# Optimization experiments

Measured on AMD Instinct MI355X. Metric: run time of the kernel, lower is better.

Reference implementation:

```python
import jax, jax.numpy as jnp
import numpy as np
from jax import lax

B, L, D, H = 2, 4096, 1024, 16
K = 4            # short conv kernel size
HD = D // H      # head dim = 64
EPS = 1e-5


def causal_dw_conv(x, w):
    # depthwise causal conv: x [B,L,D], w [D,K]
    xp = jnp.pad(x, ((0, 0), (K - 1, 0), (0, 0)))
    out = xp[:, 0:L, :] * w[:, 0]
    for j in range(1, K):
        out = out + xp[:, j:j + L, :] * w[:, j]
    return out


def setup_inputs() -> dict:
    key = jax.random.key(0)
    ks = jax.random.split(key, 10)
    s = 0.02
    return {
        "hidden_states": jax.random.normal(ks[0], (B, L, D), jnp.float32),
        "Wq": jax.random.normal(ks[1], (D, D), jnp.float32) * s,
        "Wk": jax.random.normal(ks[2], (D, D), jnp.float32) * s,
        "Wv": jax.random.normal(ks[3], (D, D), jnp.float32) * s,
        "Wb": jax.random.normal(ks[4], (D, H), jnp.float32) * s,
        "conv_q": jax.random.normal(ks[5], (D, K), jnp.float32) * s,
        "conv_k": jax.random.normal(ks[6], (D, K), jnp.float32) * s,
        "conv_v": jax.random.normal(ks[7], (D, K), jnp.float32) * s,
        "o_norm_w": jnp.ones((HD,), jnp.float32),
        "Wo": jax.random.normal(ks[8], (D, D), jnp.float32) * s,
    }


def reference(hidden_states, Wq, Wk, Wv, Wb, conv_q, conv_k, conv_v, o_norm_w, Wo):
    x = hidden_states
    # projections + short causal conv with SiLU (qk_activation == 'silu')
    q = jax.nn.silu(causal_dw_conv(x @ Wq, conv_q))
    k = jax.nn.silu(causal_dw_conv(x @ Wk, conv_k))
    v = jax.nn.silu(causal_dw_conv(x @ Wv, conv_v))

    # [B,L,D] -> [L,B,H,hd] for the time scan
    def to_heads(t):
        return t.reshape(B, L, H, HD).transpose(1, 0, 2, 3)

    q, k, v = to_heads(q), to_heads(k), to_heads(v)

    # l2 qk-norm
    q = q / jnp.linalg.norm(q, axis=-1, keepdims=True)
    k = k / jnp.linalg.norm(k, axis=-1, keepdims=True)

    # beta gate [L,B,H]
    beta = jax.nn.sigmoid(x @ Wb).transpose(1, 0, 2)

    def step(S, inp):
        qt, kt, vt, bt = inp  # [B,H,hd] x3, [B,H]
        v_old = jnp.einsum('bhk,bhkv->bhv', kt, S)
        delta = (vt - v_old) * bt[..., None]
        S = S + jnp.einsum('bhk,bhv->bhkv', kt, delta)
        ot = jnp.einsum('bhk,bhkv->bhv', qt, S)
        return S, ot

    S0 = jnp.zeros((B, H, HD, HD), x.dtype)
    _, o = lax.scan(step, S0, (q, k, v, beta))  # o: [L,B,H,hd]
    o = o.transpose(1, 0, 2, 3)  # [B,L,H,hd]

    # per-head RMSNorm
    rms = jax.lax.rsqrt(jnp.mean(o * o, axis=-1, keepdims=True) + EPS)
    o = o * rms * o_norm_w

    return o.reshape(B, L, D) @ Wo
```

## Files before the change

### kernel.cpp

```cpp
#include <hip/hip_runtime.h>
#include <hip/hip_bf16.h>
#include <math.h>

#define BB 2
#define LL 4096
#define DD 1024
#define HH 16
#define HDIM 64
#define CC 64
#define NC 64
#define BH 32
#define GG 8
#define GS 8

typedef __attribute__((ext_vector_type(8))) short short8;
typedef __attribute__((ext_vector_type(4))) float f32x4;
typedef unsigned short u16;

__device__ __forceinline__ u16 f2bf(float f) {
    unsigned int u = __float_as_uint(f);
    unsigned int r = (u + 0x7fffu + ((u >> 16) & 1u)) >> 16;
    return (u16)r;
}
__device__ __forceinline__ float bf2f(u16 h) {
    return __uint_as_float((unsigned)h << 16);
}
__device__ __forceinline__ void split2(float x, u16& h, u16& l) {
    h = f2bf(x);
    l = f2bf(x - bf2f(h));
}
__device__ __forceinline__ float4 ld_bf4(const u16* p) {
    uint2 v = *(const uint2*)p;
    return make_float4(bf2f((u16)v.x), bf2f((u16)(v.x >> 16)),
                       bf2f((u16)v.y), bf2f((u16)(v.y >> 16)));
}

__device__ __forceinline__ void gld_lds16(const void* g, void* l) {
    __builtin_amdgcn_global_load_lds(
        (const __attribute__((address_space(1))) void*)g,
        (__attribute__((address_space(3))) void*)l, 16, 0, 0);
}

__device__ __forceinline__ int swz(int r, int c) {
    return (r << 6) + ((((c >> 2) ^ (r >> 2)) & 15) << 2) + (c & 3);
}
__device__ __forceinline__ int swze(int r, int c) {
    return (r << 6) + (c ^ (((r ^ (r >> 3)) & 7) << 3));
}

__device__ __forceinline__ void mm64(const u16* __restrict__ Ah, const u16* __restrict__ Al,
                                     const u16* __restrict__ Bh, const u16* __restrict__ Bl,
                                     f32x4* acc, int w, int lane) {
    const int ln = lane & 15, kg = (lane >> 4) * 8;
#pragma unroll
    for (int kb = 0; kb < 2; ++kb) {
        const int k0 = kb * 32 + kg;
        short8 ah = *(const short8*)&Ah[swze(w * 16 + ln, k0)];
        short8 al = *(const short8*)&Al[swze(w * 16 + ln, k0)];
#pragma unroll
        for (int j = 0; j < 4; ++j) {
            short8 bh = *(const short8*)&Bh[swze(j * 16 + ln, k0)];
            short8 bl = *(const short8*)&Bl[swze(j * 16 + ln, k0)];
            acc[j] = __builtin_amdgcn_mfma_f32_16x16x32_bf16(ah, bh, acc[j], 0, 0, 0);
            acc[j] = __builtin_amdgcn_mfma_f32_16x16x32_bf16(ah, bl, acc[j], 0, 0, 0);
            acc[j] = __builtin_amdgcn_mfma_f32_16x16x32_bf16(al, bh, acc[j], 0, 0, 0);
        }
    }
}
__device__ __forceinline__ void mm64_bb(const u16* __restrict__ Ah,
                                        const u16* __restrict__ Bh,
                                        f32x4* acc, int w, int lane) {
    const int ln = lane & 15, kg = (lane >> 4) * 8;
#pragma unroll
    for (int kb = 0; kb < 2; ++kb) {
        const int k0 = kb * 32 + kg;
        short8 ah = *(const short8*)&Ah[swze(w * 16 + ln, k0)];
#pragma unroll
        for (int j = 0; j < 4; ++j) {
            short8 bh = *(const short8*)&Bh[swze(j * 16 + ln, k0)];
            acc[j] = __builtin_amdgcn_mfma_f32_16x16x32_bf16(ah, bh, acc[j], 0, 0, 0);
        }
    }
}
__device__ __forceinline__ void mm64_ab(const u16* __restrict__ Ah,
                                        const u16* __restrict__ Bh, const u16* __restrict__ Bl,
                                        f32x4* acc, int w, int lane) {
    const int ln = lane & 15, kg = (lane >> 4) * 8;
#pragma unroll
    for (int kb = 0; kb < 2; ++kb) {
        const int k0 = kb * 32 + kg;
        short8 ah = *(const short8*)&Ah[swze(w * 16 + ln, k0)];
#pragma unroll
        for (int j = 0; j < 4; ++j) {
            short8 bh = *(const short8*)&Bh[swze(j * 16 + ln, k0)];
            short8 bl = *(const short8*)&Bl[swze(j * 16 + ln, k0)];
            acc[j] = __builtin_amdgcn_mfma_f32_16x16x32_bf16(ah, bh, acc[j], 0, 0, 0);
            acc[j] = __builtin_amdgcn_mfma_f32_16x16x32_bf16(ah, bl, acc[j], 0, 0, 0);
        }
    }
}

__device__ __forceinline__ void g_to_ls(const float* __restrict__ G, u16* Ah, u16* Al, int tid) {
#pragma unroll
    for (int p = 0; p < 4; ++p) {
        int flat = p * 1024 + tid * 4;
        int r = flat >> 6, c = flat & 63;
        float4 v = *(const float4*)&G[flat];
        u16 h0, l0, h1, l1, h2, l2, h3, l3;
        split2(v.x, h0, l0); split2(v.y, h1, l1);
        split2(v.z, h2, l2); split2(v.w, h3, l3);
        int idx = swze(r, c);
        uint2 hv, lv;
        hv.x = (unsigned)h0 | ((unsigned)h1 << 16); hv.y = (unsigned)h2 | ((unsigned)h3 << 16);
        lv.x = (unsigned)l0 | ((unsigned)l1 << 16); lv.y = (unsigned)l2 | ((unsigned)l3 << 16);
        *(uint2*)&Ah[idx] = hv;
        *(uint2*)&Al[idx] = lv;
    }
}
__device__ __forceinline__ void g_to_ls_b(const u16* __restrict__ G16, u16* Ah, int tid) {
#pragma unroll
    for (int p = 0; p < 2; ++p) {
        int flat = p * 2048 + tid * 8;
        int r = flat >> 6, c = flat & 63;
        *(short8*)&Ah[swze(r, c)] = *(const short8*)&G16[flat];
    }
}

__device__ __forceinline__ void frag_to_ls(const f32x4* acc, u16* Ah, u16* Al, int w, int lane) {
    const int g = lane >> 4, ln = lane & 15;
#pragma unroll
    for (int j = 0; j < 4; ++j)
#pragma unroll
        for (int r = 0; r < 4; ++r) {
            int row = w * 16 + g * 4 + r, col = j * 16 + ln;
            u16 h, l; split2(acc[j][r], h, l);
            Ah[swze(row, col)] = h;
            Al[swze(row, col)] = l;
        }
}

__device__ __forceinline__ void g_to_frag(const float* __restrict__ G, f32x4* acc, int w, int lane) {
    const int g = lane >> 4, ln = lane & 15;
#pragma unroll
    for (int j = 0; j < 4; ++j)
#pragma unroll
        for (int r = 0; r < 4; ++r)
            acc[j][r] = G[(w * 16 + g * 4 + r) * 64 + j * 16 + ln];
}
__device__ __forceinline__ void g_add_frag(const float* __restrict__ G, f32x4* acc, int w, int lane) {
    const int g = lane >> 4, ln = lane & 15;
#pragma unroll
    for (int j = 0; j < 4; ++j)
#pragma unroll
        for (int r = 0; r < 4; ++r)
            acc[j][r] += G[(w * 16 + g * 4 + r) * 64 + j * 16 + ln];
}
__device__ __forceinline__ void frag_to_g(const f32x4* acc, float* __restrict__ G, int w, int lane) {
    const int g = lane >> 4, ln = lane & 15;
#pragma unroll
    for (int j = 0; j < 4; ++j)
#pragma unroll
        for (int r = 0; r < 4; ++r)
            G[(w * 16 + g * 4 + r) * 64 + j * 16 + ln] = acc[j][r];
}

__global__ __launch_bounds__(256) void cast_bf16_k(const float* __restrict__ in,
                                                   u16* __restrict__ out) {
    int i = (blockIdx.x * 256 + threadIdx.x) * 8;
    float4 a = *(const float4*)&in[i];
    float4 b = *(const float4*)&in[i + 4];
    uint4 o;
    o.x = (unsigned)f2bf(a.x) | ((unsigned)f2bf(a.y) << 16);
    o.y = (unsigned)f2bf(a.z) | ((unsigned)f2bf(a.w) << 16);
    o.z = (unsigned)f2bf(b.x) | ((unsigned)f2bf(b.y) << 16);
    o.w = (unsigned)f2bf(b.z) | ((unsigned)f2bf(b.w) << 16);
    *(uint4*)&out[i] = o;
}

__global__ __launch_bounds__(256) void transW4_k(const float* __restrict__ W0,
                                                 const float* __restrict__ W1,
                                                 const float* __restrict__ W2,
                                                 const float* __restrict__ W3,
                                                 u16* __restrict__ WT0) {
    __shared__ float t[32][33];
    const int which = blockIdx.z;
    const float* W = (which == 0) ? W0 : (which == 1) ? W1 : (which == 2) ? W2 : W3;
    u16* WT = WT0 + (size_t)which * 1048576;
    const int bx = blockIdx.x * 32, by = blockIdx.y * 32;
#pragma unroll
    for (int p = 0; p < 4; ++p) {
        int idx = p * 256 + threadIdx.x;
        int r = idx >> 5, cc = idx & 31;
        t[r][cc] = W[(size_t)(by + r) * 1024 + bx + cc];
    }
    __syncthreads();
#pragma unroll
    for (int p = 0; p < 4; ++p) {
        int idx = p * 256 + threadIdx.x;
        int r = idx >> 5, cc = idx & 31;
        WT[(size_t)(bx + r) * 1024 + by + cc] = f2bf(t[cc][r]);
    }
}

__device__ __forceinline__ void gemm_core(const u16* A, const u16* BT,
                                          int m0, int n0, f32x4 acc[4][4]) {
    __shared__ __align__(16) short As[128 * 32];
    __shared__ __align__(16) short Bs[128 * 32];
    const int tid = threadIdx.x;
    const int lane = tid & 63, w = tid >> 6;
    const int wr = w >> 1, wc = w & 1;
    const int ln15 = lane & 15;
    const int erow = tid >> 2;
    const int ecol = (((tid & 3) ^ ((erow >> 1) & 3)) << 3);
    const int kch = lane >> 4;
    for (int k0 = 0; k0 < 1024; k0 += 32) {
#pragma unroll
        for (int r = 0; r < 2; ++r) {
            gld_lds16(A  + (size_t)(m0 + erow + r * 64) * 1024 + k0 + ecol,
                      (short*)As + r * 2048 + tid * 8);
            gld_lds16(BT + (size_t)(n0 + erow + r * 64) * 1024 + k0 + ecol,
                      (short*)Bs + r * 2048 + tid * 8);
        }
        __syncthreads();
        short8 af[4], bf[4];
#pragma unroll
        for (int i = 0; i < 4; ++i) {
            int row = wr * 64 + i * 16 + ln15;
            af[i] = *(const short8*)&As[row * 32 + ((kch ^ ((row >> 1) & 3)) << 3)];
        }
#pragma unroll
        for (int j = 0; j < 4; ++j) {
            int row = wc * 64 + j * 16 + ln15;
            bf[j] = *(const short8*)&Bs[row * 32 + ((kch ^ ((row >> 1) & 3)) << 3)];
        }
#pragma unroll
        for (int i = 0; i < 4; ++i)
#pragma unroll
            for (int j = 0; j < 4; ++j)
                acc[i][j] = __builtin_amdgcn_mfma_f32_16x16x32_bf16(af[i], bf[j], acc[i][j], 0, 0, 0);
        __syncthreads();
    }
}

__global__ __launch_bounds__(256) void gemm_bf16(const u16* __restrict__ A,
                                                 const u16* __restrict__ BT,
                                                 float* __restrict__ C) {
    const int m0 = blockIdx.y * 128, n0 = blockIdx.x * 128;
    f32x4 acc[4][4] = {};
    gemm_core(A, BT, m0, n0, acc);
    const int lane = threadIdx.x & 63, w = threadIdx.x >> 6;
    const int crow0 = m0 + (w >> 1) * 64 + (lane >> 4) * 4;
    const int ccol0 = n0 + (w & 1) * 64 + (lane & 15);
#pragma unroll
    for (int i = 0; i < 4; ++i)
#pragma unroll
        for (int j = 0; j < 4; ++j)
#pragma unroll
            for (int r = 0; r < 4; ++r)
                C[(size_t)(crow0 + i * 16 + r) * 1024 + ccol0 + j * 16] = acc[i][j][r];
}

__global__ __launch_bounds__(256) void gemm_qkv(const u16* __restrict__ A,
                                                const u16* __restrict__ WT0,
                                                u16* __restrict__ xq16,
                                                u16* __restrict__ xk16,
                                                float* __restrict__ xv) {
    const int which = blockIdx.x >> 3;
    const int n0 = (blockIdx.x & 7) * 128;
    const int m0 = blockIdx.y * 128;
    const u16* BT = WT0 + (size_t)which * 1048576;
    f32x4 acc[4][4] = {};
    gemm_core(A, BT, m0, n0, acc);
    const int lane = threadIdx.x & 63, w = threadIdx.x >> 6;
    const int crow0 = m0 + (w >> 1) * 64 + (lane >> 4) * 4;
    const int ccol0 = n0 + (w & 1) * 64 + (lane & 15);
    if (which == 2) {
#pragma unroll
        for (int i = 0; i < 4; ++i)
#pragma unroll
            for (int j = 0; j < 4; ++j)
#pragma unroll
                for (int r = 0; r < 4; ++r)
                    xv[(size_t)(crow0 + i * 16 + r) * 1024 + ccol0 + j * 16] = acc[i][j][r];
    } else {
        u16* C16 = (which == 0) ? xq16 : xk16;
#pragma unroll
        for (int i = 0; i < 4; ++i)
#pragma unroll
            for (int j = 0; j < 4; ++j)
#pragma unroll
                for (int r = 0; r < 4; ++r)
                    C16[(size_t)(crow0 + i * 16 + r) * 1024 + ccol0 + j * 16] = f2bf(acc[i][j][r]);
    }
}

__global__ __launch_bounds__(256) void beta_k(const float* __restrict__ X,
                                              const float* __restrict__ Wb,
                                              float* __restrict__ beta) {
    int idx = blockIdx.x * 256 + threadIdx.x;
    int row = idx >> 4, h = idx & 15;
    const float* xr = X + (size_t)row * DD;
    float s = 0.f;
    for (int k4 = 0; k4 < DD; k4 += 4) {
        float4 xv = *(const float4*)&xr[k4];
        s += xv.x * Wb[(k4 + 0) * HH + h];
        s += xv.y * Wb[(k4 + 1) * HH + h];
        s += xv.z * Wb[(k4 + 2) * HH + h];
        s += xv.w * Wb[(k4 + 3) * HH + h];
    }
    float bv = 1.f / (1.f + expf(-s));
    int b = row >> 12, l = row & (LL - 1);
    beta[((size_t)b * HH + h) * LL + l] = bv;
}

__global__ __launch_bounds__(256) void conv3_k(const u16* __restrict__ xq16,
                                               const u16* __restrict__ xk16,
                                               const float* __restrict__ xv,
                                               const float* __restrict__ cwq,
                                               const float* __restrict__ cwk,
                                               const float* __restrict__ cwv,
                                               u16* __restrict__ q16,
                                               u16* __restrict__ k16,
                                               float* __restrict__ vout) {
    const int which = blockIdx.z;
    const float* cw = (which == 0) ? cwq : (which == 1) ? cwk : cwv;
    const int l0 = blockIdx.x * 16, b = blockIdx.y;
    const int tid = threadIdx.x;
    const int d0 = tid * 4;
    const float4 w0 = *(const float4*)&cw[(d0 + 0) * 4];
    const float4 w1 = *(const float4*)&cw[(d0 + 1) * 4];
    const float4 w2 = *(const float4*)&cw[(d0 + 2) * 4];
    const float4 w3 = *(const float4*)&cw[(d0 + 3) * 4];
    const int h = d0 >> 6, hd = d0 & 63;
    if (which < 2) {
        const u16* Xb = ((which == 0) ? xq16 : xk16) + (size_t)b * LL * DD;
        u16* O16 = (which == 0) ? q16 : k16;
        float4 xm3 = make_float4(0, 0, 0, 0), xm2 = xm3, xm1 = xm3;
        if (l0 > 0) {
            xm3 = ld_bf4(&Xb[(size_t)(l0 - 3) * DD + d0]);
            xm2 = ld_bf4(&Xb[(size_t)(l0 - 2) * DD + d0]);
            xm1 = ld_bf4(&Xb[(size_t)(l0 - 1) * DD + d0]);
        }
#pragma unroll
        for (int t = 0; t < 16; ++t) {
            const int l = l0 + t;
            float4 xc = ld_bf4(&Xb[(size_t)l * DD + d0]);
            float a0 = xm3.x * w0.x + xm2.x * w0.y + xm1.x * w0.z + xc.x * w0.w;
            float a1 = xm3.y * w1.x + xm2.y * w1.y + xm1.y * w1.z + xc.y * w1.w;
            float a2 = xm3.z * w2.x + xm2.z * w2.y + xm1.z * w2.z + xc.z * w2.w;
            float a3 = xm3.w * w3.x + xm2.w * w3.y + xm1.w * w3.z + xc.w * w3.w;
            a0 = a0 / (1.f + expf(-a0));
            a1 = a1 / (1.f + expf(-a1));
            a2 = a2 / (1.f + expf(-a2));
            a3 = a3 / (1.f + expf(-a3));
            float s = a0 * a0 + a1 * a1 + a2 * a2 + a3 * a3;
            s += __shfl_xor(s, 1);
            s += __shfl_xor(s, 2);
            s += __shfl_xor(s, 4);
            s += __shfl_xor(s, 8);
            float sc = rsqrtf(s);
            a0 *= sc; a1 *= sc; a2 *= sc; a3 *= sc;
            uint2 o;
            o.x = (unsigned)f2bf(a0) | ((unsigned)f2bf(a1) << 16);
            o.y = (unsigned)f2bf(a2) | ((unsigned)f2bf(a3) << 16);
            *(uint2*)&O16[(((size_t)b * HH + h) * LL + l) * 64 + hd] = o;
            xm3 = xm2; xm2 = xm1; xm1 = xc;
        }
    } else {
        const float* Xb = xv + (size_t)b * LL * DD;
        float4 xm3 = make_float4(0, 0, 0, 0), xm2 = xm3, xm1 = xm3;
        if (l0 > 0) {
            xm3 = *(const float4*)&Xb[(size_t)(l0 - 3) * DD + d0];
            xm2 = *(const float4*)&Xb[(size_t)(l0 - 2) * DD + d0];
            xm1 = *(const float4*)&Xb[(size_t)(l0 - 1) * DD + d0];
        }
#pragma unroll
        for (int t = 0; t < 16; ++t) {
            const int l = l0 + t;
            float4 xc = *(const float4*)&Xb[(size_t)l * DD + d0];
            float a0 = xm3.x * w0.x + xm2.x * w0.y + xm1.x * w0.z + xc.x * w0.w;
            float a1 = xm3.y * w1.x + xm2.y * w1.y + xm1.y * w1.z + xc.y * w1.w;
            float a2 = xm3.z * w2.x + xm2.z * w2.y + xm1.z * w2.z + xc.z * w2.w;
            float a3 = xm3.w * w3.x + xm2.w * w3.y + xm1.w * w3.z + xc.w * w3.w;
            a0 = a0 / (1.f + expf(-a0));
            a1 = a1 / (1.f + expf(-a1));
            a2 = a2 / (1.f + expf(-a2));
            a3 = a3 / (1.f + expf(-a3));
            *(float4*)&vout[(((size_t)b * HH + h) * LL + l) * 64 + hd] =
                make_float4(a0, a1, a2, a3);
            xm3 = xm2; xm2 = xm1; xm1 = xc;
        }
    }
}

__global__ __launch_bounds__(256) void phaseA5(const u16* __restrict__ kg16,
                                               const float* __restrict__ vg,
                                               const float* __restrict__ betag,
                                               float* __restrict__ Wg,
                                               float* __restrict__ UgT,
                                               float* __restrict__ Pall,
                                               float* __restrict__ BallT) {
    __shared__ __align__(16) char pool[73728];
    u16* Kh   = (u16*)pool;
    u16* KTh  = (u16*)(pool + 8192);
    float* At = (float*)(pool + 16384);
    float* WU = (float*)(pool + 32768);
    u16* WTh  = (u16*)pool;
    u16* WTl  = (u16*)(pool + 16384);
    u16* UTh  = (u16*)(pool + 24576);
    u16* UTl  = (u16*)(pool + 65536);
    float* scr = (float*)(pool + 32768);

    const int c = blockIdx.x, bh = blockIdx.y;
    const int tid = threadIdx.x, lane = tid & 63, w = tid >> 6;
    const int g = lane >> 4, ln = lane & 15;
    const int t0 = (tid >> 4) * 4, d4 = (tid & 15) * 4;
    const size_t base = ((size_t)bh * LL + (size_t)c * 64) * 64;
    const size_t obase = ((size_t)bh * NC + c) * 4096;
    const float* bet = betag + (size_t)bh * LL + (size_t)c * 64;

    g_to_ls_b(kg16 + base, Kh, tid);
    {
        u16 kv[4][4];
#pragma unroll
        for (int i = 0; i < 4; ++i) {
            uint2 v = *(const uint2*)&kg16[base + (size_t)(t0 + i) * 64 + d4];
            kv[i][0] = (u16)v.x; kv[i][1] = (u16)(v.x >> 16);
            kv[i][2] = (u16)v.y; kv[i][3] = (u16)(v.y >> 16);
        }
#pragma unroll
        for (int j = 0; j < 4; ++j) {
            uint2 hv;
            hv.x = (unsigned)kv[0][j] | ((unsigned)kv[1][j] << 16);
            hv.y = (unsigned)kv[2][j] | ((unsigned)kv[3][j] << 16);
            *(uint2*)&KTh[swze(d4 + j, t0)] = hv;
        }
    }
    __syncthreads();
    {
        f32x4 acc[4] = {};
        mm64_bb(Kh, Kh, acc, w, lane);
#pragma unroll
        for (int r = 0; r < 4; ++r) {
            int t = w * 16 + g * 4 + r;
            float bt = bet[t];
#pragma unroll
            for (int j = 0; j < 4; ++j) {
                int s = j * 16 + ln;
                At[t * 64 + s] = (s < t) ? bt * acc[j][r] : 0.f;
            }
        }
    }
#pragma unroll
    for (int p = 0; p < 8; ++p) {
        int flat = p * 1024 + tid * 4;
        int t = flat >> 7, j = flat & 127;
        float bt = bet[t];
        float4 src;
        if (j < 64) src = ld_bf4(&Kh[swze(t, j)]);
        else        src = *(const float4*)&vg[base + (size_t)t * 64 + (j - 64)];
        src.x *= bt; src.y *= bt; src.z *= bt; src.w *= bt;
        *(float4*)&WU[t * 128 + j] = src;
    }
    __syncthreads();
#pragma unroll
    for (int pb = 0; pb < 4; ++pb) {
        const int r0 = pb * 16;
        if (pb > 0) {
            const int col = tid & 127;
            const int rbase = r0 + (tid >> 7) * 8;
            float acc8[8] = {};
            for (int r = 0; r < r0; r += 4) {
                float u0 = WU[(r + 0) * 128 + col], u1 = WU[(r + 1) * 128 + col];
                float u2 = WU[(r + 2) * 128 + col], u3 = WU[(r + 3) * 128 + col];
#pragma unroll
                for (int i = 0; i < 8; ++i) {
                    float4 a4 = *(const float4*)&At[(rbase + i) * 64 + r];
                    acc8[i] += a4.x * u0 + a4.y * u1 + a4.z * u2 + a4.w * u3;
                }
            }
#pragma unroll
            for (int i = 0; i < 8; ++i) WU[(rbase + i) * 128 + col] -= acc8[i];
            __syncthreads();
        }
        if (tid < 128) {
            const int col = tid;
            float wv[16];
            wv[0] = WU[r0 * 128 + col];
#pragma unroll
            for (int t = 1; t < 16; ++t) {
                float a = WU[(r0 + t) * 128 + col];
#pragma unroll
                for (int r = 0; r < t; ++r) a -= At[(r0 + t) * 64 + r0 + r] * wv[r];
                wv[t] = a;
            }
#pragma unroll
            for (int t = 1; t < 16; ++t) WU[(r0 + t) * 128 + col] = wv[t];
        }
        __syncthreads();
    }
#pragma unroll
    for (int p = 0; p < 4; ++p) {
        int flat = p * 1024 + tid * 4;
        int t = flat >> 6, j = flat & 63;
        *(float4*)&Wg[obase + flat] = *(const float4*)&WU[t * 128 + j];
    }
    {
        u16 h4[4][4], l4[4][4];
#pragma unroll
        for (int i = 0; i < 4; ++i) {
            float4 v = *(const float4*)&WU[(t0 + i) * 128 + d4];
            split2(v.x, h4[i][0], l4[i][0]); split2(v.y, h4[i][1], l4[i][1]);
            split2(v.z, h4[i][2], l4[i][2]); split2(v.w, h4[i][3], l4[i][3]);
        }
#pragma unroll
        for (int j = 0; j < 4; ++j) {
            uint2 hv, lv;
            hv.x = (unsigned)h4[0][j] | ((unsigned)h4[1][j] << 16);
            hv.y = (unsigned)h4[2][j] | ((unsigned)h4[3][j] << 16);
            lv.x = (unsigned)l4[0][j] | ((unsigned)l4[1][j] << 16);
            lv.y = (unsigned)l4[2][j] | ((unsigned)l4[3][j] << 16);
            *(uint2*)&WTh[swze(d4 + j, t0)] = hv;
            *(uint2*)&WTl[swze(d4 + j, t0)] = lv;
        }
#pragma unroll
        for (int i = 0; i < 4; ++i) {
            float4 v = *(const float4*)&WU[(t0 + i) * 128 + 64 + d4];
            split2(v.x, h4[i][0], l4[i][0]); split2(v.y, h4[i][1], l4[i][1]);
            split2(v.z, h4[i][2], l4[i][2]); split2(v.w, h4[i][3], l4[i][3]);
        }
#pragma unroll
        for (int j = 0; j < 4; ++j) {
            uint2 hv, lv;
            hv.x = (unsigned)h4[0][j] | ((unsigned)h4[1][j] << 16);
            hv.y = (unsigned)h4[2][j] | ((unsigned)h4[3][j] << 16);
            lv.x = (unsigned)l4[0][j] | ((unsigned)l4[1][j] << 16);
            lv.y = (unsigned)l4[2][j] | ((unsigned)l4[3][j] << 16);
            *(uint2*)&UTh[swze(d4 + j, t0)] = hv;
            *(uint2*)&UTl[swze(d4 + j, t0)] = lv;
        }
    }
    __syncthreads();
#pragma unroll
    for (int p = 0; p < 4; ++p) {
        int flat = p * 1024 + tid * 4;
        int n = flat >> 6, tt = flat & 63;
        int idx = swze(n, tt);
        uint2 hh = *(const uint2*)&UTh[idx];
        uint2 ll2 = *(const uint2*)&UTl[idx];
        float4 o;
        o.x = bf2f((u16)hh.x) + bf2f((u16)ll2.x);
        o.y = bf2f((u16)(hh.x >> 16)) + bf2f((u16)(ll2.x >> 16));
        o.z = bf2f((u16)hh.y) + bf2f((u16)ll2.y);
        o.w = bf2f((u16)(hh.y >> 16)) + bf2f((u16)(ll2.y >> 16));
        *(float4*)&UgT[obase + flat] = o;
    }
    f32x4 aP[4] = {}, aB[4] = {};
    mm64_ab(KTh, WTh, WTl, aP, w, lane);
    mm64_ab(KTh, UTh, UTl, aB, w, lane);
#pragma unroll
    for (int j = 0; j < 4; ++j)
#pragma unroll
        for (int r = 0; r < 4; ++r) {
            int row = w * 16 + g * 4 + r, col = j * 16 + ln;
            float pv = ((row == col) ? 1.f : 0.f) - aP[j][r];
            Pall[obase + (size_t)row * 64 + col] = pv;
            scr[swz(row, col)] = aB[j][r];
        }
    __syncthreads();
#pragma unroll
    for (int p = 0; p < 4; ++p) {
        int flat = p * 1024 + tid * 4;
        int n = flat >> 6, dd = flat & 63;
        float4 o;
        o.x = scr[swz(dd + 0, n)];
        o.y = scr[swz(dd + 1, n)];
        o.z = scr[swz(dd + 2, n)];
        o.w = scr[swz(dd + 3, n)];
        *(float4*)&BallT[obase + flat] = o;
    }
}

__global__ __launch_bounds__(256) void compose3(const float* __restrict__ Pall,
                                                const float* __restrict__ BallT,
                                                float* __restrict__ Pg,
                                                float* __restrict__ BgT) {
    __shared__ __align__(16) char pool[81920];
    u16* Ph = (u16*)pool;
    u16* Pl = (u16*)(pool + 8192);
    u16* Bh = (u16*)(pool + 16384);
    u16* Bl = (u16*)(pool + 24576);
    u16* nh = (u16*)(pool + 32768);
    u16* nl = (u16*)(pool + 40960);
    float* scr = (float*)(pool + 49152);
    const int g = blockIdx.x, bh = blockIdx.y;
    const int tid = threadIdx.x, lane = tid & 63, w = tid >> 6;
    const int gi = lane >> 4, ln = lane & 15;
    const size_t base0 = ((size_t)bh * NC + (size_t)g * GS) * 4096;
    f32x4 mP[4], mB[4];
#pragma unroll
    for (int p = 0; p < 4; ++p) {
        int flat = p * 1024 + tid * 4;
        int r = flat >> 6, c4 = flat & 63;
        *(float4*)&scr[swz(r, c4)] = *(const float4*)&Pall[base0 + flat];
    }
    g_to_frag(BallT + base0, mB, w, lane);
    __syncthreads();
#pragma unroll
    for (int j = 0; j < 4; ++j)
#pragma unroll
        for (int r = 0; r < 4; ++r) {
            int row = w * 16 + gi * 4 + r, col = j * 16 + ln;
            mP[j][r] = scr[swz(col, row)];
        }
    for (int s = 1; s < GS; ++s) {
        __syncthreads();
        frag_to_ls(mP, Ph, Pl, w, lane);
        frag_to_ls(mB, Bh, Bl, w, lane);
        g_to_ls(&Pall[base0 + (size_t)s * 4096], nh, nl, tid);
        __syncthreads();
        f32x4 aP[4] = {}, aB[4] = {};
        mm64(Ph, Pl, nh, nl, aP, w, lane);
        mm64(Bh, Bl, nh, nl, aB, w, lane);
        g_add_frag(&BallT[base0 + (size_t)s * 4096], aB, w, lane);
#pragma unroll
        for (int j = 0; j < 4; ++j) { mP[j] = aP[j]; mB[j] = aB[j]; }
    }
    const size_t gbase = ((size_t)bh * GG + g) * 4096;
    frag_to_g(mB, BgT + gbase, w, lane);
    __syncthreads();
#pragma unroll
    for (int j = 0; j < 4; ++j)
#pragma unroll
        for (int r = 0; r < 4; ++r) {
            int row = w * 16 + gi * 4 + r, col = j * 16 + ln;
            scr[swz(row, col)] = mP[j][r];
        }
    __syncthreads();
#pragma unroll
    for (int p = 0; p < 4; ++p) {
        int flat = p * 1024 + tid * 4;
        int a = flat >> 6, b0 = flat & 63;
        float4 o;
        o.x = scr[swz(b0 + 0, a)];
        o.y = scr[swz(b0 + 1, a)];
        o.z = scr[swz(b0 + 2, a)];
        o.w = scr[swz(b0 + 3, a)];
        *(float4*)&Pg[gbase + flat] = o;
    }
}

__global__ __launch_bounds__(256) void scanG3(const float* __restrict__ Pg,
                                              const float* __restrict__ BgT,
                                              float* __restrict__ SallT) {
    __shared__ __align__(16) char pool[32768];
    u16* Sh = (u16*)pool;
    u16* Sl = (u16*)(pool + 8192);
    u16* nh = (u16*)(pool + 16384);
    u16* nl = (u16*)(pool + 24576);
    const int bh = blockIdx.x;
    const int tid = threadIdx.x, lane = tid & 63, w = tid >> 6;
    f32x4 mS[4] = {};
    for (int g = 0; g < GG; ++g) {
        const size_t sbase = ((size_t)bh * NC + (size_t)g * GS) * 4096;
        frag_to_g(mS, SallT + sbase, w, lane);
        if (g == GG - 1) break;
        __syncthreads();
        frag_to_ls(mS, Sh, Sl, w, lane);
        g_to_ls(&Pg[((size_t)bh * GG + g) * 4096], nh, nl, tid);
        __syncthreads();
        f32x4 a[4] = {};
        mm64(Sh, Sl, nh, nl, a, w, lane);
        g_add_frag(&BgT[((size_t)bh * GG + g) * 4096], a, w, lane);
#pragma unroll
        for (int j = 0; j < 4; ++j) mS[j] = a[j];
    }
}

__global__ __launch_bounds__(256) void rollout3(const float* __restrict__ Pall,
                                                const float* __restrict__ BallT,
                                                float* __restrict__ SallT) {
    __shared__ __align__(16) char pool[32768];
    u16* Sh = (u16*)pool;
    u16* Sl = (u16*)(pool + 8192);
    u16* nh = (u16*)(pool + 16384);
    u16* nl = (u16*)(pool + 24576);
    const int g = blockIdx.x, bh = blockIdx.y;
    const int tid = threadIdx.x, lane = tid & 63, w = tid >> 6;
    const size_t base0 = ((size_t)bh * NC + (size_t)g * GS) * 4096;
    f32x4 mS[4];
    g_to_frag(SallT + base0, mS, w, lane);
    for (int j = 1; j < GS; ++j) {
        __syncthreads();
        frag_to_ls(mS, Sh, Sl, w, lane);
        g_to_ls(&Pall[base0 + (size_t)(j - 1) * 4096], nh, nl, tid);
        __syncthreads();
        f32x4 a[4] = {};
        mm64(Sh, Sl, nh, nl, a, w, lane);
        g_add_frag(&BallT[base0 + (size_t)(j - 1) * 4096], a, w, lane);
#pragma unroll
        for (int jj = 0; jj < 4; ++jj) mS[jj] = a[jj];
        frag_to_g(mS, SallT + base0 + (size_t)j * 4096, w, lane);
    }
}

__global__ __launch_bounds__(256) void phaseO4(const float* __restrict__ Wg,
                                               const float* __restrict__ UgT,
                                               const u16* __restrict__ qg16,
                                               const u16* __restrict__ kg16,
                                               const float* __restrict__ SallT,
                                               const float* __restrict__ nw,
                                               u16* __restrict__ ob) {
    __shared__ __align__(16) char pool[57344];
    u16* Qh = (u16*)pool;
    u16* Kh = (u16*)(pool + 8192);
    u16* Wh = (u16*)(pool + 16384);
    u16* Wl = (u16*)(pool + 24576);
    u16* Sh = (u16*)(pool + 32768);
    u16* Sl = (u16*)(pool + 40960);
    u16* Dl = (u16*)(pool + 49152);
    u16* Dh = Kh;
    u16* Mh = Wh; u16* Ml = Wl;
    const int c = blockIdx.x, bh = blockIdx.y;
    const int b = bh >> 4, h = bh & 15;
    const int tid = threadIdx.x, lane = tid & 63, w = tid >> 6;
    const int gi = lane >> 4, ln = lane & 15;
    const size_t tbase = ((size_t)bh * NC + c) * 4096;
    const size_t qkbase = ((size_t)bh * LL + (size_t)c * 64) * 64;
    g_to_ls_b(qg16 + qkbase, Qh, tid);
    g_to_ls_b(kg16 + qkbase, Kh, tid);
    g_to_ls(&Wg[tbase], Wh, Wl, tid);
    g_to_ls(&SallT[tbase], Sh, Sl, tid);
    __syncthreads();
    f32x4 aM[4] = {}, aD[4] = {};
    mm64_bb(Qh, Kh, aM, w, lane);
    mm64(Sh, Sl, Wh, Wl, aD, w, lane);
    __syncthreads();
#pragma unroll
    for (int j = 0; j < 4; ++j)
#pragma unroll
        for (int r = 0; r < 4; ++r) {
            int row = w * 16 + gi * 4 + r, col = j * 16 + ln;
            float mv = (col <= row) ? aM[j][r] : 0.f;
            u16 mh_, ml_; split2(mv, mh_, ml_);
            Mh[swze(row, col)] = mh_;
            Ml[swze(row, col)] = ml_;
            float dv = UgT[tbase + (size_t)row * 64 + col] - aD[j][r];
            u16 dh_, dl_; split2(dv, dh_, dl_);
            Dh[swze(row, col)] = dh_;
            Dl[swze(row, col)] = dl_;
        }
    __syncthreads();
    f32x4 aO[4] = {};
    mm64_ab(Qh, Sh, Sl, aO, w, lane);
    mm64(Mh, Ml, Dh, Dl, aO, w, lane);
    float nwv[4];
#pragma unroll
    for (int j = 0; j < 4; ++j) nwv[j] = nw[j * 16 + ln];
#pragma unroll
    for (int r = 0; r < 4; ++r) {
        float ss = 0.f;
#pragma unroll
        for (int j = 0; j < 4; ++j) ss += aO[j][r] * aO[j][r];
        ss += __shfl_xor(ss, 1);
        ss += __shfl_xor(ss, 2);
        ss += __shfl_xor(ss, 4);
        ss += __shfl_xor(ss, 8);
        float rms = rsqrtf(ss * (1.f / 64.f) + 1e-5f);
        int row = w * 16 + gi * 4 + r;
        size_t orow = ((size_t)b * LL + (size_t)c * 64 + row) * DD + (size_t)h * 64;
#pragma unroll
        for (int j = 0; j < 4; ++j)
            ob[orow + j * 16 + ln] = f2bf(aO[j][r] * rms * nwv[j]);
    }
}

extern "C" void kernel_launch(void* const* d_in, const int* in_sizes, int n_in,
                              void* d_out, int out_size, void* d_ws, size_t ws_size,
                              hipStream_t stream) {
    const float* x  = (const float*)d_in[0];
    const float* Wq = (const float*)d_in[1];
    const float* Wk = (const float*)d_in[2];
    const float* Wv = (const float*)d_in[3];
    const float* Wb = (const float*)d_in[4];
    const float* cq = (const float*)d_in[5];
    const float* ck = (const float*)d_in[6];
    const float* cv = (const float*)d_in[7];
    const float* nw = (const float*)d_in[8];
    const float* Wo = (const float*)d_in[9];
    float* out = (float*)d_out;
    float* ws = (float*)d_ws;

    const size_t SZ = (size_t)BB * LL * DD;
    float* xv    = ws;
    float* v     = ws + SZ;
    float* Wg    = ws + 2 * SZ;
    float* UgT   = ws + 3 * SZ;
    float* SallT = ws + 4 * SZ;
    u16* xb   = (u16*)(ws + 5 * SZ);
    u16* q16  = xb;
    u16* xq16 = (u16*)(ws + 5 * SZ) + SZ;
    u16* xk16 = (u16*)(ws + 5 * SZ) + 2 * SZ;
    u16* k16  = (u16*)(ws + 5 * SZ) + 3 * SZ;
    float* beta = ws + 7 * SZ;
    u16* wqT  = (u16*)(beta + (size_t)BH * LL);
    float* PgB = (float*)(wqT + (size_t)4 * 1048576);
    float* BgT = PgB + 1048576;

    float* Pall  = xv;
    float* BallT = out;
    u16* ob   = (u16*)v;
    u16* woT  = wqT + (size_t)3 * 1048576;

    dim3 blk(256);

    cast_bf16_k<<<dim3(4096), blk, 0, stream>>>(x, xb);
    transW4_k<<<dim3(32, 32, 4), blk, 0, stream>>>(Wq, Wk, Wv, Wo, wqT);
    gemm_qkv<<<dim3(24, 64), blk, 0, stream>>>(xb, wqT, xq16, xk16, xv);
    beta_k<<<dim3(512), blk, 0, stream>>>(x, Wb, beta);
    conv3_k<<<dim3(LL / 16, BB, 3), blk, 0, stream>>>(xq16, xk16, xv, cq, ck, cv, q16, k16, v);
    phaseA5<<<dim3(NC, BH), blk, 0, stream>>>(k16, v, beta, Wg, UgT, Pall, BallT);
    compose3<<<dim3(GG, BH), blk, 0, stream>>>(Pall, BallT, PgB, BgT);
    scanG3<<<dim3(BH), blk, 0, stream>>>(PgB, BgT, SallT);
    rollout3<<<dim3(GG, BH), blk, 0, stream>>>(Pall, BallT, SallT);
    phaseO4<<<dim3(NC, BH), blk, 0, stream>>>(Wg, UgT, q16, k16, SallT, nw, ob);
    gemm_bf16<<<dim3(8, 64), blk, 0, stream>>>(ob, woT, out);
}
```

Baseline: 363.1 us.

## Double-buffer LDS tiles in bf16 GEMM core to overlap loads with MFMA

```diff
diff --git a/kernel.cpp b/kernel.cpp
--- a/kernel.cpp
+++ b/kernel.cpp
@@ -204,8 +204,8 @@
 
 __device__ __forceinline__ void gemm_core(const u16* A, const u16* BT,
                                           int m0, int n0, f32x4 acc[4][4]) {
-    __shared__ __align__(16) short As[128 * 32];
-    __shared__ __align__(16) short Bs[128 * 32];
+    __shared__ __align__(16) short As[2][128 * 32];
+    __shared__ __align__(16) short Bs[2][128 * 32];
     const int tid = threadIdx.x;
     const int lane = tid & 63, w = tid >> 6;
     const int wr = w >> 1, wc = w & 1;
@@ -213,33 +213,58 @@
     const int erow = tid >> 2;
     const int ecol = (((tid & 3) ^ ((erow >> 1) & 3)) << 3);
     const int kch = lane >> 4;
-    for (int k0 = 0; k0 < 1024; k0 += 32) {
-#pragma unroll
-        for (int r = 0; r < 2; ++r) {
-            gld_lds16(A  + (size_t)(m0 + erow + r * 64) * 1024 + k0 + ecol,
-                      (short*)As + r * 2048 + tid * 8);
-            gld_lds16(BT + (size_t)(n0 + erow + r * 64) * 1024 + k0 + ecol,
-                      (short*)Bs + r * 2048 + tid * 8);
-        }
-        __syncthreads();
-        short8 af[4], bf[4];
-#pragma unroll
-        for (int i = 0; i < 4; ++i) {
-            int row = wr * 64 + i * 16 + ln15;
-            af[i] = *(const short8*)&As[row * 32 + ((kch ^ ((row >> 1) & 3)) << 3)];
-        }
-#pragma unroll
-        for (int j = 0; j < 4; ++j) {
-            int row = wc * 64 + j * 16 + ln15;
-            bf[j] = *(const short8*)&Bs[row * 32 + ((kch ^ ((row >> 1) & 3)) << 3)];
-        }
-#pragma unroll
-        for (int i = 0; i < 4; ++i)
-#pragma unroll
-            for (int j = 0; j < 4; ++j)
-                acc[i][j] = __builtin_amdgcn_mfma_f32_16x16x32_bf16(af[i], bf[j], acc[i][j], 0, 0, 0);
-        __syncthreads();
-    }
+
+#define STAGE(buf, k0)                                                        \
+    {                                                                         \
+        _Pragma("unroll")                                                     \
+        for (int r = 0; r < 2; ++r) {                                         \
+            gld_lds16(A  + (size_t)(m0 + erow + r * 64) * 1024 + (k0) + ecol, \
+                      (short*)As[buf] + r * 2048 + tid * 8);                  \
+            gld_lds16(BT + (size_t)(n0 + erow + r * 64) * 1024 + (k0) + ecol, \
+                      (short*)Bs[buf] + r * 2048 + tid * 8);                  \
+        }                                                                     \
+    }
+
+#define COMPUTE(buf)                                                           \
+    {                                                                          \
+        short8 af[4], bf[4];                                                   \
+        _Pragma("unroll")                                                      \
+        for (int i = 0; i < 4; ++i) {                                          \
+            int row = wr * 64 + i * 16 + ln15;                                 \
+            af[i] = *(const short8*)&As[buf][row * 32 + ((kch ^ ((row >> 1) & 3)) << 3)]; \
+        }                                                                      \
+        _Pragma("unroll")                                                      \
+        for (int j = 0; j < 4; ++j) {                                          \
+            int row = wc * 64 + j * 16 + ln15;                                 \
+            bf[j] = *(const short8*)&Bs[buf][row * 32 + ((kch ^ ((row >> 1) & 3)) << 3)]; \
+        }                                                                      \
+        __builtin_amdgcn_s_setprio(1);                                         \
+        _Pragma("unroll")                                                      \
+        for (int i = 0; i < 4; ++i)                                            \
+            _Pragma("unroll")                                                  \
+            for (int j = 0; j < 4; ++j)                                        \
+                acc[i][j] = __builtin_amdgcn_mfma_f32_16x16x32_bf16(af[i], bf[j], acc[i][j], 0, 0, 0); \
+        __builtin_amdgcn_s_setprio(0);                                         \
+    }
+
+    STAGE(0, 0);
+    for (int t = 0; t < 31; ++t) {
+        const int cur = t & 1;
+        STAGE(cur ^ 1, (t + 1) * 32);
+        asm volatile("s_waitcnt vmcnt(4)" ::: "memory");
+        __builtin_amdgcn_sched_barrier(0);
+        __builtin_amdgcn_s_barrier();
+        COMPUTE(cur);
+        asm volatile("s_waitcnt lgkmcnt(0)" ::: "memory");
+        __builtin_amdgcn_sched_barrier(0);
+        __builtin_amdgcn_s_barrier();
+    }
+    asm volatile("s_waitcnt vmcnt(0)" ::: "memory");
+    __builtin_amdgcn_sched_barrier(0);
+    __builtin_amdgcn_s_barrier();
+    COMPUTE(1);
+#undef STAGE
+#undef COMPUTE
 }
 
 __global__ __launch_bounds__(256) void gemm_bf16(const u16* __restrict__ A,
```

Measured after the change: 364.8 us. No clear change (+0.5%).
